# Optimization experiments

Measured on AMD Instinct MI355X. Metric: run time of the kernel, lower is better.

The kernel has to match this reference:

```python
import jax, jax.numpy as jnp
import numpy as np
import math

D_MODEL = 1024
N_HEADS = 16
D_K = D_MODEL // N_HEADS
HIDDEN = 4096
R_SOFTPLUS_0 = 1.442695041
EPS = 1e-6


def setup_inputs() -> dict:
    key = jax.random.key(0)
    ks = jax.random.split(key, 16)
    B, S = 4, 2048
    s = 0.02
    inp = {
        "inputs": jax.random.normal(ks[0], (B, S, D_MODEL), jnp.float32),
        "mask": jnp.zeros((1, 1, S, S), jnp.float32),
        # RmsNorm (direct_scale=True -> init 1.0)
        "rms_scale": jnp.ones((D_MODEL,), jnp.float32),
        # attention projections (torch Linear: y = x @ W.T + b)
        "Wq": jax.random.normal(ks[1], (D_MODEL, D_MODEL), jnp.float32) * s,
        "bq": jnp.zeros((D_MODEL,), jnp.float32),
        "Wk": jax.random.normal(ks[2], (D_MODEL, D_MODEL), jnp.float32) * s,
        "bk": jnp.zeros((D_MODEL,), jnp.float32),
        "Wv": jax.random.normal(ks[3], (D_MODEL, D_MODEL), jnp.float32) * s,
        "bv": jnp.zeros((D_MODEL,), jnp.float32),
        "per_dim_scale": jnp.zeros((D_K,), jnp.float32),
        "Wpost": jax.random.normal(ks[4], (D_MODEL, D_MODEL), jnp.float32) * s,
        "bpost": jnp.zeros((D_MODEL,), jnp.float32),
        # FFN LayerNorm (direct_scale=False -> scale param init 0, effective 1+scale)
        "ln_scale": jnp.zeros((D_MODEL,), jnp.float32),
        "ln_bias": jnp.zeros((D_MODEL,), jnp.float32),
        "W1": jax.random.normal(ks[5], (HIDDEN, D_MODEL), jnp.float32) * s,
        "b1": jnp.zeros((HIDDEN,), jnp.float32),
        "W2": jax.random.normal(ks[6], (D_MODEL, HIDDEN), jnp.float32) * s,
        "b2": jnp.zeros((D_MODEL,), jnp.float32),
    }
    return inp


def _rms_norm(x, scale):
    ms = jnp.mean(x * x, axis=-1, keepdims=True)
    return x * jax.lax.rsqrt(ms + EPS) * scale


def _layer_norm(x, scale, bias):
    mean = jnp.mean(x, axis=-1, keepdims=True)
    var = jnp.mean((x - mean) ** 2, axis=-1, keepdims=True)
    return (x - mean) * jax.lax.rsqrt(var + EPS) * (1.0 + scale) + bias


def reference(inputs, mask, rms_scale, Wq, bq, Wk, bk, Wv, bv, per_dim_scale,
              Wpost, bpost, ln_scale, ln_bias, W1, b1, W2, b2):
    B, S, _ = inputs.shape
    x = _rms_norm(inputs, rms_scale)
    # projections -> [B, H, S, Dk]
    def split_heads(t):
        return t.reshape(B, S, N_HEADS, D_K).transpose(0, 2, 1, 3)
    q = split_heads(x @ Wq.T + bq)
    k = split_heads(x @ Wk.T + bk)
    v = split_heads(x @ Wv.T + bv)
    # PerDimScale: (r_softplus_0 / sqrt(d_k)) * softplus(param)
    scale = (R_SOFTPLUS_0 / math.sqrt(D_K)) * jax.nn.softplus(per_dim_scale)
    q = q * scale
    attn = jnp.einsum("bhqd,bhkd->bhqk", q, k) + mask
    attn = jax.nn.softmax(attn, axis=-1)
    out = jnp.einsum("bhqk,bhkd->bhqd", attn, v)
    out = out.transpose(0, 2, 1, 3).reshape(B, S, D_MODEL)
    attn_out = out @ Wpost.T + bpost
    h = attn_out + inputs  # residual (dropout=0)
    # FeedForward with pre-LayerNorm and residual
    y = _layer_norm(h, ln_scale, ln_bias)
    y = jax.nn.relu(y @ W1.T + b1)
    y = y @ W2.T + b2
    return y + h
```

## Files before the change

kernel.cpp:

```cpp
#include <hip/hip_runtime.h>
#include <hip/hip_bf16.h>

typedef unsigned short u16;
typedef __attribute__((ext_vector_type(8))) short short8;
typedef __attribute__((ext_vector_type(4))) float floatx4;

#define R_PDS 0.18033688f
#define LOG2E 1.4426950408889634f

__device__ __forceinline__ float bf2f(u16 u) {
    union { float f; unsigned int i; } c; c.i = ((unsigned int)u) << 16; return c.f;
}
__device__ __forceinline__ u16 f2b(float f) {
    union { float f; unsigned int i; } c; c.f = f;
    unsigned int r = c.i + 0x7fffu + ((c.i >> 16) & 1u);
    return (u16)(r >> 16);
}
__device__ __forceinline__ unsigned int pk2(float a, float b) {
    __hip_bfloat162 h = __float22bfloat162_rn(float2{a, b});
    unsigned int u; __builtin_memcpy(&u, &h, 4); return u;
}

__device__ __forceinline__ void async16(const u16* g, u16* l) {
    __builtin_amdgcn_global_load_lds(
        (const __attribute__((address_space(1))) unsigned int*)g,
        (__attribute__((address_space(3))) unsigned int*)l, 16, 0, 0);
}

__global__ __launch_bounds__(256) void f2b_all_k(const float* __restrict__ Wq, const float* __restrict__ Wk,
                                                 const float* __restrict__ Wv, const float* __restrict__ Wp,
                                                 const float* __restrict__ W1, const float* __restrict__ W2,
                                                 u16* __restrict__ Wqkvb, u16* __restrict__ Wpb,
                                                 u16* __restrict__ W1b,  u16* __restrict__ W2b,
                                                 int* flag) {
    int bid = blockIdx.x;
    if (bid == 0 && threadIdx.x == 0) *flag = 0;
    const float* src; u16* dst; int off;
    if      (bid < 1024) { src = Wq; dst = Wqkvb;                off = bid; }
    else if (bid < 2048) { src = Wk; dst = Wqkvb + 1024 * 1024;  off = bid - 1024; }
    else if (bid < 3072) { src = Wv; dst = Wqkvb + 2048 * 1024;  off = bid - 2048; }
    else if (bid < 4096) { src = Wp; dst = Wpb;                  off = bid - 3072; }
    else if (bid < 8192) { src = W1; dst = W1b;                  off = bid - 4096; }
    else                 { src = W2; dst = W2b;                  off = bid - 8192; }
    int i = off * 256 + threadIdx.x;
    float4 v = ((const float4*)src)[i];
    uint2 w; w.x = pk2(v.x, v.y); w.y = pk2(v.z, v.w);
    ((uint2*)dst)[i] = w;
}

__global__ __launch_bounds__(256) void mask_any_k(const float* __restrict__ mask, int* flag) {
    int i = blockIdx.x * 256 + threadIdx.x;
    uint4 u = ((const uint4*)mask)[i];
    unsigned int v = (u.x | u.y | u.z | u.w) & 0x7fffffffu;
    if (v) atomicOr(flag, 1);
}

__global__ __launch_bounds__(256) void rmsnorm_k(const float* __restrict__ in,
                                                 const float* __restrict__ gscale,
                                                 u16* __restrict__ out) {
    int row = blockIdx.x;
    int t = threadIdx.x, lane = t & 63, wave = t >> 6;
    const float* x = in + (size_t)row * 1024;
    float4 v = *(const float4*)(x + t * 4);
    float ss = v.x*v.x + v.y*v.y + v.z*v.z + v.w*v.w;
    for (int o = 1; o < 64; o <<= 1) ss += __shfl_xor(ss, o, 64);
    __shared__ float red[4];
    if (lane == 0) red[wave] = ss;
    __syncthreads();
    float tot = red[0] + red[1] + red[2] + red[3];
    float inv = rsqrtf(tot * (1.0f / 1024.0f) + 1e-6f);
    float4 s = *(const float4*)(gscale + t * 4);
    uint2 w;
    w.x = pk2(v.x * inv * s.x, v.y * inv * s.y);
    w.y = pk2(v.z * inv * s.z, v.w * inv * s.w);
    *(uint2*)(out + (size_t)row * 1024 + t * 4) = w;
}

__global__ __launch_bounds__(256) void layernorm_k(const u16* __restrict__ in,
                                                   const float* __restrict__ gs,
                                                   const float* __restrict__ gb,
                                                   u16* __restrict__ out) {
    int row = blockIdx.x;
    int t = threadIdx.x, lane = t & 63, wave = t >> 6;
    const u16* x = in + (size_t)row * 1024;
    uint2 u = *(const uint2*)(x + t * 4);
    float v0 = bf2f((u16)(u.x & 0xffff)), v1 = bf2f((u16)(u.x >> 16));
    float v2 = bf2f((u16)(u.y & 0xffff)), v3 = bf2f((u16)(u.y >> 16));
    float s1 = v0 + v1 + v2 + v3;
    float s2 = v0*v0 + v1*v1 + v2*v2 + v3*v3;
    for (int o = 1; o < 64; o <<= 1) { s1 += __shfl_xor(s1, o, 64); s2 += __shfl_xor(s2, o, 64); }
    __shared__ float r1[4], r2[4];
    if (lane == 0) { r1[wave] = s1; r2[wave] = s2; }
    __syncthreads();
    float mean = (r1[0] + r1[1] + r1[2] + r1[3]) * (1.0f / 1024.0f);
    float var  = (r2[0] + r2[1] + r2[2] + r2[3]) * (1.0f / 1024.0f) - mean * mean;
    var = fmaxf(var, 0.0f);
    float inv = rsqrtf(var + 1e-6f);
    float4 sc = *(const float4*)(gs + t * 4);
    float4 bb = *(const float4*)(gb + t * 4);
    uint2 w;
    w.x = pk2((v0 - mean) * inv * (1.0f + sc.x) + bb.x,
              (v1 - mean) * inv * (1.0f + sc.y) + bb.y);
    w.y = pk2((v2 - mean) * inv * (1.0f + sc.z) + bb.z,
              (v3 - mean) * inv * (1.0f + sc.w) + bb.w);
    *(uint2*)(out + (size_t)row * 1024 + t * 4) = w;
}

__device__ __forceinline__ void xcd_swizzle(int& bx, int& by) {
    int gx = gridDim.x, nwg = gx * gridDim.y;
    int lin = blockIdx.y * gx + blockIdx.x;
    int swz = (lin & 7) * (nwg >> 3) + (lin >> 3);
    bx = swz % gx; by = swz / gx;
}

__device__ __forceinline__ void gemm8_core(const u16* __restrict__ A, const u16* __restrict__ B,
                                           int K, int NG, int m0, int n0,
                                           u16* lds, floatx4 (&acc)[8][4]) {
    const int t = threadIdx.x, wave = t >> 6, lane = t & 63;
    const int quad = lane >> 4, ln = lane & 15;
    const int wave_m = wave >> 2, wave_n = wave & 3;

    const int rowS = t >> 3;
    const int srcb = ((t & 7) * 16) ^ (((t >> 3) & 7) << 4);
    const u16* Ab = A + (size_t)(m0 + rowS) * K + (srcb >> 1);
    const u16* Bb = B + (size_t)(n0 + rowS) * K + (srcb >> 1);
    const size_t rstep = (size_t)64 * K;
    const size_t hstep = (size_t)128 * K;
    const int ldw = wave * 512;

    #define STAGE_A8(buf, h, kt) do { \
        u16* _l = lds + (buf) * 32768 + (h) * 8192 + ldw; \
        const u16* _g = Ab + (size_t)(h) * hstep + (kt); \
        async16(_g, _l); async16(_g + rstep, _l + 4096); } while (0)
    #define STAGE_B8(buf, h, kt) do { \
        u16* _l = lds + (buf) * 32768 + 16384 + (h) * 8192 + ldw; \
        const u16* _g = Bb + (size_t)(h) * hstep + (kt); \
        async16(_g, _l); async16(_g + rstep, _l + 4096); } while (0)

    #define RD8(base, lr, ks) \
        (*(const short8*)((base) + (lr) * 64 + ((((ks) * 64 + quad * 16) ^ (((lr) & 7) << 4)) >> 1)))

    STAGE_B8(0, 0, 0); STAGE_B8(0, 1, 0);
    STAGE_A8(0, 0, 0); STAGE_A8(0, 1, 0);
    if (NG > 1) {
        STAGE_B8(1, 0, 64); STAGE_B8(1, 1, 64);
        asm volatile("s_waitcnt vmcnt(4)" ::: "memory");
    } else {
        asm volatile("s_waitcnt vmcnt(0)" ::: "memory");
    }
    __builtin_amdgcn_s_barrier();

    for (int g = 0; g < NG; ++g) {
        const int cur = g & 1;
        const u16* aH = lds + cur * 32768 + wave_m * 8192;
        const u16* bH = lds + cur * 32768 + 16384 + (wave_n >> 1) * 8192;
        const int lrB = (wave_n & 1) * 64;
        short8 bf[4][2];
        #pragma unroll
        for (int q = 0; q < 4; ++q) {
            short8 af[2][2];
            #pragma unroll
            for (int mt = 0; mt < 2; ++mt)
                #pragma unroll
                for (int ks = 0; ks < 2; ++ks)
                    af[mt][ks] = RD8(aH, q * 32 + mt * 16 + ln, ks);
            if (q == 0) {
                #pragma unroll
                for (int nt = 0; nt < 4; ++nt)
                    #pragma unroll
                    for (int ks = 0; ks < 2; ++ks)
                        bf[nt][ks] = RD8(bH, lrB + nt * 16 + ln, ks);
            }
            if (q == 0 && g + 1 < NG) STAGE_A8(cur ^ 1, 0, (g + 1) * 64);
            if (q == 1 && g + 1 < NG) STAGE_A8(cur ^ 1, 1, (g + 1) * 64);
            if (q == 2 && g + 2 < NG) STAGE_B8(cur, 0, (g + 2) * 64);
            if (q == 3 && g + 2 < NG) STAGE_B8(cur, 1, (g + 2) * 64);
            __builtin_amdgcn_s_barrier();
            asm volatile("s_waitcnt lgkmcnt(0)" ::: "memory");
            __builtin_amdgcn_sched_barrier(0);
            __builtin_amdgcn_s_setprio(1);
            #pragma unroll
            for (int ks = 0; ks < 2; ++ks)
                #pragma unroll
                for (int mt = 0; mt < 2; ++mt)
                    #pragma unroll
                    for (int nt = 0; nt < 4; ++nt)
                        acc[q * 2 + mt][nt] = __builtin_amdgcn_mfma_f32_16x16x32_bf16(
                            af[mt][ks], bf[nt][ks], acc[q * 2 + mt][nt], 0, 0, 0);
            __builtin_amdgcn_s_setprio(0);
            __builtin_amdgcn_sched_barrier(0);
            if (q == 3 && g + 1 < NG) {
                if (g + 2 < NG) asm volatile("s_waitcnt vmcnt(4)" ::: "memory");
                else            asm volatile("s_waitcnt vmcnt(0)" ::: "memory");
            }
            __builtin_amdgcn_s_barrier();
        }
    }
    #undef STAGE_A8
    #undef STAGE_B8
    #undef RD8
}

__device__ __forceinline__ void gemm8h_core(const u16* __restrict__ A, const u16* __restrict__ B,
                                            int K, int NG, int m0, int n0,
                                            u16* lds, floatx4 (&acc)[4][4]) {
    const int t = threadIdx.x, wave = t >> 6, lane = t & 63;
    const int quad = lane >> 4, ln = lane & 15;
    const int wm = (wave >> 2) * 64, wn = (wave & 3) * 64;

    const int rowS = t >> 3;
    const int srcb = ((t & 7) * 16) ^ (((t >> 3) & 7) << 4);
    const u16* Ab = A + (size_t)(m0 + rowS) * K + (srcb >> 1);
    const u16* Bb = B + (size_t)(n0 + rowS) * K + (srcb >> 1);
    const size_t hstep = (size_t)64 * K;
    const int ldw = wave * 512;

    #define STAGE_AH(buf, h, kt) \
        async16(Ab + (size_t)(h) * hstep + (kt), lds + (buf) * 24576 + (h) * 4096 + ldw)
    #define STAGE_BH(buf, h, kt) \
        async16(Bb + (size_t)(h) * hstep + (kt), lds + (buf) * 24576 + 8192 + (h) * 4096 + ldw)
    #define RD8H(base, lr, ks) \
        (*(const short8*)((base) + (lr) * 64 + ((((ks) * 64 + quad * 16) ^ (((lr) & 7) << 4)) >> 1)))

    STAGE_BH(0, 0, 0); STAGE_BH(0, 1, 0); STAGE_BH(0, 2, 0); STAGE_BH(0, 3, 0);
    STAGE_AH(0, 0, 0); STAGE_AH(0, 1, 0);
    if (NG > 1) {
        STAGE_BH(1, 0, 64); STAGE_BH(1, 1, 64); STAGE_BH(1, 2, 64); STAGE_BH(1, 3, 64);
        asm volatile("s_waitcnt vmcnt(4)" ::: "memory");
    } else {
        asm volatile("s_waitcnt vmcnt(0)" ::: "memory");
    }
    __builtin_amdgcn_s_barrier();

    for (int g = 0; g < NG; ++g) {
        const int cur = g & 1;
        const u16* aB = lds + cur * 24576;
        const u16* bB = lds + cur * 24576 + 8192;
        short8 bf[4][2];
        #pragma unroll
        for (int q = 0; q < 2; ++q) {
            short8 af[2][2];
            #pragma unroll
            for (int mt = 0; mt < 2; ++mt)
                #pragma unroll
                for (int ks = 0; ks < 2; ++ks)
                    af[mt][ks] = RD8H(aB, wm + (q * 2 + mt) * 16 + ln, ks);
            if (q == 0) {
                #pragma unroll
                for (int nt = 0; nt < 4; ++nt)
                    #pragma unroll
                    for (int ks = 0; ks < 2; ++ks)
                        bf[nt][ks] = RD8H(bB, wn + nt * 16 + ln, ks);
            }
            if (q == 0 && g + 1 < NG) {
                STAGE_AH(cur ^ 1, 0, (g + 1) * 64); STAGE_AH(cur ^ 1, 1, (g + 1) * 64);
            }
            if (q == 1 && g + 2 < NG) {
                STAGE_BH(cur, 0, (g + 2) * 64); STAGE_BH(cur, 1, (g + 2) * 64);
                STAGE_BH(cur, 2, (g + 2) * 64); STAGE_BH(cur, 3, (g + 2) * 64);
            }
            __builtin_amdgcn_s_barrier();
            asm volatile("s_waitcnt lgkmcnt(0)" ::: "memory");
            __builtin_amdgcn_sched_barrier(0);
            __builtin_amdgcn_s_setprio(1);
            #pragma unroll
            for (int ks = 0; ks < 2; ++ks)
                #pragma unroll
                for (int mt = 0; mt < 2; ++mt)
                    #pragma unroll
                    for (int nt = 0; nt < 4; ++nt)
                        acc[q * 2 + mt][nt] = __builtin_amdgcn_mfma_f32_16x16x32_bf16(
                            af[mt][ks], bf[nt][ks], acc[q * 2 + mt][nt], 0, 0, 0);
            __builtin_amdgcn_s_setprio(0);
            __builtin_amdgcn_sched_barrier(0);
            if (q == 1 && g + 1 < NG) {
                if (g + 2 < NG) asm volatile("s_waitcnt vmcnt(4)" ::: "memory");
                else            asm volatile("s_waitcnt vmcnt(0)" ::: "memory");
            }
            __builtin_amdgcn_s_barrier();
        }
    }
    #undef STAGE_AH
    #undef STAGE_BH
    #undef RD8H
}

template <int EPI, bool OUTF32, bool RESF32>
__global__ __launch_bounds__(512, 2) void gemm8_bt_k(const u16* __restrict__ A,
                                                     const u16* __restrict__ B,
                                                     const float* __restrict__ bias,
                                                     const void* __restrict__ res,
                                                     void* __restrict__ Cv,
                                                     int M, int N, int K) {
    __shared__ __align__(16) u16 lds[65536];
    int bx, by; xcd_swizzle(bx, by);
    const int m0 = by * 256, n0 = bx * 256;
    const int t = threadIdx.x, wave = t >> 6, lane = t & 63;
    const int quad = lane >> 4, ln = lane & 15;
    const int wm = (wave >> 2) * 128, wn = (wave & 3) * 64;

    floatx4 acc[8][4];
    #pragma unroll
    for (int mf = 0; mf < 8; mf++)
        #pragma unroll
        for (int nf = 0; nf < 4; nf++) acc[mf][nf] = (floatx4)0.0f;

    gemm8_core(A, B, K, K >> 6, m0, n0, lds, acc);

    #pragma unroll
    for (int nf = 0; nf < 4; nf++) {
        int col = n0 + wn + nf * 16 + ln;
        float bv = bias[col];
        #pragma unroll
        for (int mf = 0; mf < 8; mf++) {
            int row = m0 + wm + mf * 16 + quad * 4;
            #pragma unroll
            for (int r = 0; r < 4; r++) {
                float v = acc[mf][nf][r] + bv;
                if (EPI == 1) v = fmaxf(v, 0.0f);
                if (EPI == 2) {
                    if (RESF32) v += ((const float*)res)[(size_t)(row + r) * N + col];
                    else        v += bf2f(((const u16*)res)[(size_t)(row + r) * N + col]);
                }
                if (OUTF32) ((float*)Cv)[(size_t)(row + r) * N + col] = v;
                else        ((u16*)Cv)[(size_t)(row + r) * N + col] = f2b(v);
            }
        }
    }
}

template <int EPI, bool OUTF32, bool RESF32>
__global__ __launch_bounds__(512, 2) void gemm8h_bt_k(const u16* __restrict__ A,
                                                      const u16* __restrict__ B,
                                                      const float* __restrict__ bias,
                                                      const void* __restrict__ res,
                                                      void* __restrict__ Cv,
                                                      int M, int N, int K) {
    __shared__ __align__(16) u16 lds[49152];
    int bx, by; xcd_swizzle(bx, by);
    const int m0 = by * 128, n0 = bx * 256;
    const int t = threadIdx.x, wave = t >> 6, lane = t & 63;
    const int quad = lane >> 4, ln = lane & 15;
    const int wm = (wave >> 2) * 64, wn = (wave & 3) * 64;

    floatx4 acc[4][4];
    #pragma unroll
    for (int mf = 0; mf < 4; mf++)
        #pragma unroll
        for (int nf = 0; nf < 4; nf++) acc[mf][nf] = (floatx4)0.0f;

    gemm8h_core(A, B, K, K >> 6, m0, n0, lds, acc);

    #pragma unroll
    for (int nf = 0; nf < 4; nf++) {
        int col = n0 + wn + nf * 16 + ln;
        float bv = bias[col];
        #pragma unroll
        for (int mf = 0; mf < 4; mf++) {
            int row = m0 + wm + mf * 16 + quad * 4;
            #pragma unroll
            for (int r = 0; r < 4; r++) {
                float v = acc[mf][nf][r] + bv;
                if (EPI == 1) v = fmaxf(v, 0.0f);
                if (EPI == 2) {
                    if (RESF32) v += ((const float*)res)[(size_t)(row + r) * N + col];
                    else        v += bf2f(((const u16*)res)[(size_t)(row + r) * N + col]);
                }
                if (OUTF32) ((float*)Cv)[(size_t)(row + r) * N + col] = v;
                else        ((u16*)Cv)[(size_t)(row + r) * N + col] = f2b(v);
            }
        }
    }
}

__global__ __launch_bounds__(512, 2) void gemm8h_qkv_k(const u16* __restrict__ A,
                                                       const u16* __restrict__ B,
                                                       const float* __restrict__ bq,
                                                       const float* __restrict__ bk,
                                                       const float* __restrict__ bv,
                                                       const float* __restrict__ pds,
                                                       u16* __restrict__ C) {
    const int K = 1024, N = 3072;
    __shared__ __align__(16) u16 lds[49152];
    int bx, by; xcd_swizzle(bx, by);
    const int m0 = by * 128, n0 = bx * 256;
    const int t = threadIdx.x, wave = t >> 6, lane = t & 63;
    const int quad = lane >> 4, ln = lane & 15;
    const int wm = (wave >> 2) * 64, wn = (wave & 3) * 64;

    floatx4 acc[4][4];
    #pragma unroll
    for (int mf = 0; mf < 4; mf++)
        #pragma unroll
        for (int nf = 0; nf < 4; nf++) acc[mf][nf] = (floatx4)0.0f;

    gemm8h_core(A, B, K, K >> 6, m0, n0, lds, acc);

    #pragma unroll
    for (int nf = 0; nf < 4; nf++) {
        int col = n0 + wn + nf * 16 + ln;
        float bv_, sc = 1.0f;
        if (col < 1024) {
            bv_ = bq[col];
            float xp = pds[col & 63];
            float sp = (xp > 20.0f) ? xp : log1pf(__expf(xp));
            sc = R_PDS * sp * LOG2E;
        } else if (col < 2048) bv_ = bk[col - 1024];
        else                   bv_ = bv[col - 2048];
        #pragma unroll
        for (int mf = 0; mf < 4; mf++) {
            int row = m0 + wm + mf * 16 + quad * 4;
            #pragma unroll
            for (int r = 0; r < 4; r++)
                C[(size_t)(row + r) * N + col] = f2b((acc[mf][nf][r] + bv_) * sc);
        }
    }
}

__global__ __launch_bounds__(256) void transpose_v_k(const u16* __restrict__ qkv, u16* __restrict__ vT) {
    __shared__ u16 tile[64][65];
    int st = blockIdx.x, bh = blockIdx.y;
    int b = bh >> 4, h = bh & 15;
    const u16* vb = qkv + (size_t)(b * 2048 + st * 64) * 3072 + 2048 + h * 64;
    int t = threadIdx.x;
    for (int i = t; i < 4096; i += 256) {
        int s = i >> 6, d = i & 63;
        tile[s][d] = vb[(size_t)s * 3072 + d];
    }
    __syncthreads();
    u16* ob = vT + (size_t)bh * 131072 + st * 64;
    for (int i = t; i < 4096; i += 256) {
        int d = i >> 6, s = i & 63;
        ob[(size_t)d * 2048 + s] = tile[s][d];
    }
}

__global__ __launch_bounds__(256, 2) void attn_k(const u16* __restrict__ qkv,
                                                 const u16* __restrict__ vT,
                                                 const float* __restrict__ mask,
                                                 const int* __restrict__ flag,
                                                 u16* __restrict__ o) {
    __shared__ __align__(16) u16 QPs[256 * 64];
    __shared__ __align__(16) u16 Ks[64 * 64];
    __shared__ __align__(16) u16 Vs[64 * 64];

    const int t = threadIdx.x, wave = t >> 6, lane = t & 63;
    const int quad = lane >> 4, ln = lane & 15;
    const int lin = blockIdx.y * 8 + blockIdx.x;
    const int qt = (lin >> 3) & 7;
    const int bh = ((lin & 7) << 3) | (lin >> 6);
    const int b = bh >> 4, h = bh & 15;
    const int q0 = qt * 256;
    const int wm = wave * 64;

    const u16* qb = qkv + (size_t)(b * 2048 + q0) * 3072 + h * 64;
    #pragma unroll
    for (int i = 0; i < 8; i++) {
        int c = t + i * 256;
        int row = c >> 3, seg = c & 7;
        int byt = (seg * 16) ^ ((row & 7) << 4);
        *(uint4*)&QPs[row * 64 + (byt >> 1)] = *(const uint4*)(qb + (size_t)row * 3072 + seg * 8);
    }
    __syncthreads();

    short8 qf[4][2];
    #pragma unroll
    for (int mt = 0; mt < 4; mt++)
        #pragma unroll
        for (int ks = 0; ks < 2; ks++) {
            int row = wm + mt * 16 + ln;
            int byt = (ks * 64 + quad * 16) ^ ((ln & 7) << 4);
            qf[mt][ks] = *(const short8*)&QPs[row * 64 + (byt >> 1)];
        }

    short8 ones_f;
    #pragma unroll
    for (int i = 0; i < 8; i++) ones_f[i] = (short)0x3F80;

    floatx4 acc_o[4][4], acc_l[4];
    #pragma unroll
    for (int mt = 0; mt < 4; mt++) {
        acc_l[mt] = (floatx4)0.0f;
        #pragma unroll
        for (int dt = 0; dt < 4; dt++) acc_o[mt][dt] = (floatx4)0.0f;
    }

    const int mflag = *flag;
    const u16* kb = qkv + (size_t)(b * 2048) * 3072 + 1024 + h * 64;
    const u16* vg = vT + (size_t)bh * 131072;

    const int r0 = t >> 3, sseg = t & 7;
    const int wofs = (((sseg * 16) ^ ((r0 & 7) << 4)) >> 1);
    const int s0 = sseg * 8;
    const u16* kp0 = kb + (size_t)r0 * 3072 + s0;
    const u16* kp1 = kb + (size_t)(r0 + 32) * 3072 + s0;
    const u16* vp0 = vg + (size_t)r0 * 2048 + s0;
    const u16* vp1 = vg + (size_t)(r0 + 32) * 2048 + s0;

    uint4 kr0 = *(const uint4*)(kp0);
    uint4 kr1 = *(const uint4*)(kp1);
    uint4 vr0 = *(const uint4*)(vp0);
    uint4 vr1 = *(const uint4*)(vp1);

    for (int kv0 = 0; kv0 < 2048; kv0 += 64) {
        __syncthreads();
        *(uint4*)&Ks[r0 * 64 + wofs]        = kr0;
        *(uint4*)&Ks[(r0 + 32) * 64 + wofs] = kr1;
        *(uint4*)&Vs[r0 * 64 + wofs]        = vr0;
        *(uint4*)&Vs[(r0 + 32) * 64 + wofs] = vr1;
        __syncthreads();
        if (kv0 + 64 < 2048) {
            size_t ko = (size_t)(kv0 + 64) * 3072;
            int    vo = kv0 + 64;
            kr0 = *(const uint4*)(kp0 + ko);
            kr1 = *(const uint4*)(kp1 + ko);
            vr0 = *(const uint4*)(vp0 + vo);
            vr1 = *(const uint4*)(vp1 + vo);
        }

        #pragma unroll
        for (int nt = 0; nt < 4; nt++) {
            floatx4 sa[4];
            #pragma unroll
            for (int mt = 0; mt < 4; mt++) sa[mt] = (floatx4)0.0f;
            #pragma unroll
            for (int ks = 0; ks < 2; ks++) {
                int byt = (ks * 64 + quad * 16) ^ ((ln & 7) << 4);
                short8 kf = *(const short8*)&Ks[(nt * 16 + ln) * 64 + (byt >> 1)];
                #pragma unroll
                for (int mt = 0; mt < 4; mt++)
                    sa[mt] = __builtin_amdgcn_mfma_f32_16x16x32_bf16(kf, qf[mt][ks], sa[mt], 0, 0, 0);
            }
            if (mflag) {
                #pragma unroll
                for (int mt = 0; mt < 4; mt++)
                    #pragma unroll
                    for (int r = 0; r < 4; r++) {
                        int kc = kv0 + nt * 16 + quad * 4 + r;
                        sa[mt][r] += mask[(size_t)(q0 + wm + mt * 16 + ln) * 2048 + kc] * LOG2E;
                    }
            }
            #pragma unroll
            for (int mt = 0; mt < 4; mt++) {
                uint2 w;
                w.x = pk2(__builtin_amdgcn_exp2f(fminf(sa[mt][0], 80.0f)),
                          __builtin_amdgcn_exp2f(fminf(sa[mt][1], 80.0f)));
                w.y = pk2(__builtin_amdgcn_exp2f(fminf(sa[mt][2], 80.0f)),
                          __builtin_amdgcn_exp2f(fminf(sa[mt][3], 80.0f)));
                int row = wm + mt * 16 + ln;
                int byt = (nt * 32 + quad * 8) ^ ((ln & 7) << 4);
                *(uint2*)&QPs[row * 64 + (byt >> 1)] = w;
            }
        }

        #pragma unroll
        for (int ks = 0; ks < 2; ks++) {
            short8 a[4];
            #pragma unroll
            for (int mt = 0; mt < 4; mt++) {
                int row = wm + mt * 16 + ln;
                int byt = (ks * 64 + quad * 16) ^ ((ln & 7) << 4);
                a[mt] = *(const short8*)&QPs[row * 64 + (byt >> 1)];
            }
            #pragma unroll
            for (int mt = 0; mt < 4; mt++)
                acc_l[mt] = __builtin_amdgcn_mfma_f32_16x16x32_bf16(a[mt], ones_f, acc_l[mt], 0, 0, 0);
            #pragma unroll
            for (int dt = 0; dt < 4; dt++) {
                int byt = (ks * 64 + quad * 16) ^ ((ln & 7) << 4);
                short8 bfr = *(const short8*)&Vs[(dt * 16 + ln) * 64 + (byt >> 1)];
                #pragma unroll
                for (int mt = 0; mt < 4; mt++)
                    acc_o[mt][dt] = __builtin_amdgcn_mfma_f32_16x16x32_bf16(a[mt], bfr, acc_o[mt][dt], 0, 0, 0);
            }
        }
    }

    u16* ob = o + (size_t)(b * 2048 + q0) * 1024 + h * 64;
    #pragma unroll
    for (int mt = 0; mt < 4; mt++) {
        #pragma unroll
        for (int r = 0; r < 4; r++) {
            float inv = 1.0f / acc_l[mt][r];
            int row = wm + mt * 16 + quad * 4 + r;
            #pragma unroll
            for (int dt = 0; dt < 4; dt++)
                ob[(size_t)row * 1024 + dt * 16 + ln] = f2b(acc_o[mt][dt][r] * inv);
        }
    }
}

extern "C" void kernel_launch(void* const* d_in, const int* in_sizes, int n_in,
                              void* d_out, int out_size, void* d_ws, size_t ws_size,
                              hipStream_t stream) {
    const float* inp    = (const float*)d_in[0];
    const float* mask   = (const float*)d_in[1];
    const float* rms_s  = (const float*)d_in[2];
    const float* Wq     = (const float*)d_in[3];
    const float* bq     = (const float*)d_in[4];
    const float* Wk     = (const float*)d_in[5];
    const float* bk     = (const float*)d_in[6];
    const float* Wv     = (const float*)d_in[7];
    const float* bv     = (const float*)d_in[8];
    const float* pds    = (const float*)d_in[9];
    const float* Wpost  = (const float*)d_in[10];
    const float* bpost  = (const float*)d_in[11];
    const float* ln_s   = (const float*)d_in[12];
    const float* ln_b   = (const float*)d_in[13];
    const float* W1     = (const float*)d_in[14];
    const float* b1     = (const float*)d_in[15];
    const float* W2     = (const float*)d_in[16];
    const float* b2     = (const float*)d_in[17];
    float* out = (float*)d_out;

    char* w = (char*)d_ws;
    const size_t MB = 1u << 20;
    u16* W1b   = (u16*)(w + 0 * MB);
    u16* W2b   = (u16*)(w + 8 * MB);
    u16* qkv   = (u16*)(w + 16 * MB);
    u16* x     = (u16*)(w + 64 * MB);
    u16* o     = (u16*)(w + 64 * MB);
    u16* Wqkvb = (u16*)(w + 80 * MB);
    u16* Wpb   = (u16*)(w + 86 * MB);
    u16* yln   = (u16*)(w + 80 * MB);
    u16* vT    = (u16*)(w + 96 * MB);
    u16* hb    = (u16*)(w + 96 * MB);
    u16* f1    = (u16*)(w + 16 * MB);
    int* flag  = (int*)(w + 112 * MB);

    f2b_all_k<<<12288, 256, 0, stream>>>(Wq, Wk, Wv, Wpost, W1, W2, Wqkvb, Wpb, W1b, W2b, flag);
    mask_any_k<<<4096, 256, 0, stream>>>(mask, flag);

    rmsnorm_k<<<8192, 256, 0, stream>>>(inp, rms_s, x);

    gemm8h_qkv_k<<<dim3(12, 64), 512, 0, stream>>>(x, Wqkvb, bq, bk, bv, pds, qkv);

    transpose_v_k<<<dim3(32, 64), 256, 0, stream>>>(qkv, vT);

    attn_k<<<dim3(8, 64), 256, 0, stream>>>(qkv, vT, mask, flag, o);

    gemm8h_bt_k<2, false, true><<<dim3(4, 64), 512, 0, stream>>>(o, Wpb, bpost, inp, hb, 8192, 1024, 1024);

    layernorm_k<<<8192, 256, 0, stream>>>(hb, ln_s, ln_b, yln);

    gemm8_bt_k<1, false, true><<<dim3(16, 32), 512, 0, stream>>>(yln, W1b, b1, nullptr, f1, 8192, 4096, 1024);
    gemm8h_bt_k<2, true, false><<<dim3(4, 64), 512, 0, stream>>>(f1, W2b, b2, hb, out, 8192, 1024, 4096);
}
```

Measured before the change: 506.2 us.

## Double-buffer K/V tiles in attention kernel with single barrier per tile

```diff
diff --git a/kernel.cpp b/kernel.cpp
--- a/kernel.cpp
+++ b/kernel.cpp
@@ -440,9 +440,9 @@
                                                  const float* __restrict__ mask,
                                                  const int* __restrict__ flag,
                                                  u16* __restrict__ o) {
-    __shared__ __align__(16) u16 QPs[256 * 64];
-    __shared__ __align__(16) u16 Ks[64 * 64];
-    __shared__ __align__(16) u16 Vs[64 * 64];
+    __shared__ __align__(16) u16 QPs[16384];
+    __shared__ __align__(16) u16 Ksh[8192];
+    __shared__ __align__(16) u16 Vsh[8192];
 
     const int t = threadIdx.x, wave = t >> 6, lane = t & 63;
     const int quad = lane >> 4, ln = lane & 15;
@@ -453,128 +453,151 @@
     const int q0 = qt * 256;
     const int wm = wave * 64;
 
+    const int m_swz = (ln & 7) << 4;
+    const int o_k0 = ln * 128 + ((quad * 16) ^ m_swz);
+    const int o_k1 = ln * 128 + ((64 + quad * 16) ^ m_swz);
+    const int o_q0 = (wm + ln) * 128 + ((quad * 16) ^ m_swz);
+    const int o_q1 = (wm + ln) * 128 + ((64 + quad * 16) ^ m_swz);
+    int o_p[4];
+    #pragma unroll
+    for (int nt = 0; nt < 4; nt++)
+        o_p[nt] = (wm + ln) * 128 + (((nt * 32 + quad * 8) ^ m_swz));
+
+    #define RD8AT(arr, byteoff) (*(const short8*)((const char*)(arr) + (byteoff)))
+
     const u16* qb = qkv + (size_t)(b * 2048 + q0) * 3072 + h * 64;
     #pragma unroll
     for (int i = 0; i < 8; i++) {
         int c = t + i * 256;
         int row = c >> 3, seg = c & 7;
-        int byt = (seg * 16) ^ ((row & 7) << 4);
-        *(uint4*)&QPs[row * 64 + (byt >> 1)] = *(const uint4*)(qb + (size_t)row * 3072 + seg * 8);
-    }
-    __syncthreads();
-
-    short8 qf[4][2];
-    #pragma unroll
-    for (int mt = 0; mt < 4; mt++)
-        #pragma unroll
-        for (int ks = 0; ks < 2; ks++) {
-            int row = wm + mt * 16 + ln;
-            int byt = (ks * 64 + quad * 16) ^ ((ln & 7) << 4);
-            qf[mt][ks] = *(const short8*)&QPs[row * 64 + (byt >> 1)];
-        }
-
-    short8 ones_f;
-    #pragma unroll
-    for (int i = 0; i < 8; i++) ones_f[i] = (short)0x3F80;
-
-    floatx4 acc_o[4][4], acc_l[4];
-    #pragma unroll
-    for (int mt = 0; mt < 4; mt++) {
-        acc_l[mt] = (floatx4)0.0f;
-        #pragma unroll
-        for (int dt = 0; dt < 4; dt++) acc_o[mt][dt] = (floatx4)0.0f;
-    }
-
-    const int mflag = *flag;
+        int gs = (seg ^ (row & 7)) * 8;
+        *(uint4*)&QPs[c * 8] = *(const uint4*)(qb + (size_t)row * 3072 + gs);
+    }
+
+    const int r0 = t >> 3, sseg = t & 7;
+    const int s0 = (sseg ^ (r0 & 7)) * 8;
     const u16* kb = qkv + (size_t)(b * 2048) * 3072 + 1024 + h * 64;
     const u16* vg = vT + (size_t)bh * 131072;
-
-    const int r0 = t >> 3, sseg = t & 7;
-    const int wofs = (((sseg * 16) ^ ((r0 & 7) << 4)) >> 1);
-    const int s0 = sseg * 8;
     const u16* kp0 = kb + (size_t)r0 * 3072 + s0;
     const u16* kp1 = kb + (size_t)(r0 + 32) * 3072 + s0;
     const u16* vp0 = vg + (size_t)r0 * 2048 + s0;
     const u16* vp1 = vg + (size_t)(r0 + 32) * 2048 + s0;
-
-    uint4 kr0 = *(const uint4*)(kp0);
-    uint4 kr1 = *(const uint4*)(kp1);
-    uint4 vr0 = *(const uint4*)(vp0);
-    uint4 vr1 = *(const uint4*)(vp1);
-
-    for (int kv0 = 0; kv0 < 2048; kv0 += 64) {
+    const size_t KST = (size_t)64 * 3072;
+
+    {
+        uint4 k0 = *(const uint4*)kp0, k1 = *(const uint4*)kp1;
+        uint4 v0 = *(const uint4*)vp0, v1 = *(const uint4*)vp1;
+        kp0 += KST; kp1 += KST; vp0 += 64; vp1 += 64;
+        *(uint4*)&Ksh[t * 8]        = k0;
+        *(uint4*)&Ksh[2048 + t * 8] = k1;
+        *(uint4*)&Vsh[t * 8]        = v0;
+        *(uint4*)&Vsh[2048 + t * 8] = v1;
+    }
+    __syncthreads();
+
+    short8 qf[4][2];
+    #pragma unroll
+    for (int mt = 0; mt < 4; mt++) {
+        qf[mt][0] = RD8AT(QPs, o_q0 + mt * 2048);
+        qf[mt][1] = RD8AT(QPs, o_q1 + mt * 2048);
+    }
+
+    short8 ones_f;
+    #pragma unroll
+    for (int i = 0; i < 8; i++) ones_f[i] = (short)0x3F80;
+
+    floatx4 acc_o[4][4], acc_l[4];
+    #pragma unroll
+    for (int mt = 0; mt < 4; mt++) {
+        acc_l[mt] = (floatx4)0.0f;
+        #pragma unroll
+        for (int dt = 0; dt < 4; dt++) acc_o[mt][dt] = (floatx4)0.0f;
+    }
+
+    const int mflag = *flag;
+    int kvbase = 0;
+
+    #define COMPUTE(BUF) do {                                                              \
+        _Pragma("unroll")                                                                  \
+        for (int nt = 0; nt < 4; nt++) {                                                   \
+            floatx4 sa[4];                                                                 \
+            _Pragma("unroll")                                                              \
+            for (int mt = 0; mt < 4; mt++) sa[mt] = (floatx4)0.0f;                         \
+            short8 kf0 = RD8AT(Ksh, o_k0 + (BUF) * 8192 + nt * 2048);                      \
+            short8 kf1 = RD8AT(Ksh, o_k1 + (BUF) * 8192 + nt * 2048);                      \
+            _Pragma("unroll")                                                              \
+            for (int mt = 0; mt < 4; mt++) {                                               \
+                sa[mt] = __builtin_amdgcn_mfma_f32_16x16x32_bf16(kf0, qf[mt][0], sa[mt], 0, 0, 0); \
+                sa[mt] = __builtin_amdgcn_mfma_f32_16x16x32_bf16(kf1, qf[mt][1], sa[mt], 0, 0, 0); \
+            }                                                                              \
+            if (mflag) {                                                                   \
+                _Pragma("unroll")                                                          \
+                for (int mt = 0; mt < 4; mt++)                                             \
+                    _Pragma("unroll")                                                      \
+                    for (int r = 0; r < 4; r++) {                                          \
+                        int kc = kvbase + nt * 16 + quad * 4 + r;                          \
+                        sa[mt][r] += mask[(size_t)(q0 + wm + mt * 16 + ln) * 2048 + kc] * LOG2E; \
+                    }                                                                      \
+            }                                                                              \
+            _Pragma("unroll")                                                              \
+            for (int mt = 0; mt < 4; mt++) {                                               \
+                uint2 w;                                                                   \
+                w.x = pk2(__builtin_amdgcn_exp2f(fminf(sa[mt][0], 80.0f)),                 \
+                          __builtin_amdgcn_exp2f(fminf(sa[mt][1], 80.0f)));                \
+                w.y = pk2(__builtin_amdgcn_exp2f(fminf(sa[mt][2], 80.0f)),                 \
+                          __builtin_amdgcn_exp2f(fminf(sa[mt][3], 80.0f)));                \
+                *(uint2*)((char*)QPs + o_p[nt] + mt * 2048) = w;                           \
+            }                                                                              \
+        }                                                                                  \
+        _Pragma("unroll")                                                                  \
+        for (int ks = 0; ks < 2; ks++) {                                                   \
+            const int oq = ks ? o_q1 : o_q0;                                               \
+            const int ov = ks ? o_k1 : o_k0;                                               \
+            short8 a[4];                                                                   \
+            _Pragma("unroll")                                                              \
+            for (int mt = 0; mt < 4; mt++) a[mt] = RD8AT(QPs, oq + mt * 2048);             \
+            _Pragma("unroll")                                                              \
+            for (int mt = 0; mt < 4; mt++)                                                 \
+                acc_l[mt] = __builtin_amdgcn_mfma_f32_16x16x32_bf16(a[mt], ones_f, acc_l[mt], 0, 0, 0); \
+            _Pragma("unroll")                                                              \
+            for (int dt = 0; dt < 4; dt++) {                                               \
+                short8 bfr = RD8AT(Vsh, ov + (BUF) * 8192 + dt * 2048);                    \
+                _Pragma("unroll")                                                          \
+                for (int mt = 0; mt < 4; mt++)                                             \
+                    acc_o[mt][dt] = __builtin_amdgcn_mfma_f32_16x16x32_bf16(a[mt], bfr, acc_o[mt][dt], 0, 0, 0); \
+            }                                                                              \
+        }                                                                                  \
+    } while (0)
+
+    #pragma unroll 1
+    for (int it = 0; it < 16; ++it) {
+        uint4 k0 = *(const uint4*)kp0, k1 = *(const uint4*)kp1;
+        uint4 v0 = *(const uint4*)vp0, v1 = *(const uint4*)vp1;
+        kp0 += KST; kp1 += KST; vp0 += 64; vp1 += 64;
+        COMPUTE(0);
+        *(uint4*)&Ksh[4096 + t * 8]        = k0;
+        *(uint4*)&Ksh[4096 + 2048 + t * 8] = k1;
+        *(uint4*)&Vsh[4096 + t * 8]        = v0;
+        *(uint4*)&Vsh[4096 + 2048 + t * 8] = v1;
         __syncthreads();
-        *(uint4*)&Ks[r0 * 64 + wofs]        = kr0;
-        *(uint4*)&Ks[(r0 + 32) * 64 + wofs] = kr1;
-        *(uint4*)&Vs[r0 * 64 + wofs]        = vr0;
-        *(uint4*)&Vs[(r0 + 32) * 64 + wofs] = vr1;
-        __syncthreads();
-        if (kv0 + 64 < 2048) {
-            size_t ko = (size_t)(kv0 + 64) * 3072;
-            int    vo = kv0 + 64;
-            kr0 = *(const uint4*)(kp0 + ko);
-            kr1 = *(const uint4*)(kp1 + ko);
-            vr0 = *(const uint4*)(vp0 + vo);
-            vr1 = *(const uint4*)(vp1 + vo);
-        }
-
-        #pragma unroll
-        for (int nt = 0; nt < 4; nt++) {
-            floatx4 sa[4];
-            #pragma unroll
-            for (int mt = 0; mt < 4; mt++) sa[mt] = (floatx4)0.0f;
-            #pragma unroll
-            for (int ks = 0; ks < 2; ks++) {
-                int byt = (ks * 64 + quad * 16) ^ ((ln & 7) << 4);
-                short8 kf = *(const short8*)&Ks[(nt * 16 + ln) * 64 + (byt >> 1)];
-                #pragma unroll
-                for (int mt = 0; mt < 4; mt++)
-                    sa[mt] = __builtin_amdgcn_mfma_f32_16x16x32_bf16(kf, qf[mt][ks], sa[mt], 0, 0, 0);
-            }
-            if (mflag) {
-                #pragma unroll
-                for (int mt = 0; mt < 4; mt++)
-                    #pragma unroll
-                    for (int r = 0; r < 4; r++) {
-                        int kc = kv0 + nt * 16 + quad * 4 + r;
-                        sa[mt][r] += mask[(size_t)(q0 + wm + mt * 16 + ln) * 2048 + kc] * LOG2E;
-                    }
-            }
-            #pragma unroll
-            for (int mt = 0; mt < 4; mt++) {
-                uint2 w;
-                w.x = pk2(__builtin_amdgcn_exp2f(fminf(sa[mt][0], 80.0f)),
-                          __builtin_amdgcn_exp2f(fminf(sa[mt][1], 80.0f)));
-                w.y = pk2(__builtin_amdgcn_exp2f(fminf(sa[mt][2], 80.0f)),
-                          __builtin_amdgcn_exp2f(fminf(sa[mt][3], 80.0f)));
-                int row = wm + mt * 16 + ln;
-                int byt = (nt * 32 + quad * 8) ^ ((ln & 7) << 4);
-                *(uint2*)&QPs[row * 64 + (byt >> 1)] = w;
-            }
-        }
-
-        #pragma unroll
-        for (int ks = 0; ks < 2; ks++) {
-            short8 a[4];
-            #pragma unroll
-            for (int mt = 0; mt < 4; mt++) {
-                int row = wm + mt * 16 + ln;
-                int byt = (ks * 64 + quad * 16) ^ ((ln & 7) << 4);
-                a[mt] = *(const short8*)&QPs[row * 64 + (byt >> 1)];
-            }
-            #pragma unroll
-            for (int mt = 0; mt < 4; mt++)
-                acc_l[mt] = __builtin_amdgcn_mfma_f32_16x16x32_bf16(a[mt], ones_f, acc_l[mt], 0, 0, 0);
-            #pragma unroll
-            for (int dt = 0; dt < 4; dt++) {
-                int byt = (ks * 64 + quad * 16) ^ ((ln & 7) << 4);
-                short8 bfr = *(const short8*)&Vs[(dt * 16 + ln) * 64 + (byt >> 1)];
-                #pragma unroll
-                for (int mt = 0; mt < 4; mt++)
-                    acc_o[mt][dt] = __builtin_amdgcn_mfma_f32_16x16x32_bf16(a[mt], bfr, acc_o[mt][dt], 0, 0, 0);
-            }
-        }
-    }
+        kvbase += 64;
+        if (it < 15) {
+            k0 = *(const uint4*)kp0; k1 = *(const uint4*)kp1;
+            v0 = *(const uint4*)vp0; v1 = *(const uint4*)vp1;
+            kp0 += KST; kp1 += KST; vp0 += 64; vp1 += 64;
+        }
+        COMPUTE(1);
+        if (it < 15) {
+            *(uint4*)&Ksh[t * 8]        = k0;
+            *(uint4*)&Ksh[2048 + t * 8] = k1;
+            *(uint4*)&Vsh[t * 8]        = v0;
+            *(uint4*)&Vsh[2048 + t * 8] = v1;
+            __syncthreads();
+        }
+        kvbase += 64;
+    }
+    #undef COMPUTE
+    #undef RD8AT
 
     u16* ob = o + (size_t)(b * 2048 + q0) * 1024 + h * 64;
     #pragma unroll
```

Result: slower. 518.4 us (+2.4%).
